# Optimization experiments

Hardware: AMD Instinct MI355X
Metric: run time of the kernel (lower is better)

Reference implementation:

```python
import jax, jax.numpy as jnp
import numpy as np

B, N, DIM = 8, 1024, 1024
HEADS, DIM_HEAD = 16, 64
INNER = HEADS * DIM_HEAD  # 1024


def setup_inputs() -> dict:
    key = jax.random.key(0)
    k1, k2, k3 = jax.random.split(key, 3)
    x = jax.random.normal(k1, (B, N, DIM), dtype=jnp.float32)
    # Dense kernels (Glorot-ish scale for numerical sanity)
    w_qkv = jax.random.normal(k2, (DIM, 3 * INNER), dtype=jnp.float32) * (DIM ** -0.5)
    w_out = jax.random.normal(k3, (INNER, DIM), dtype=jnp.float32) * (INNER ** -0.5)
    b_out = jnp.zeros((DIM,), dtype=jnp.float32)
    return {"x": x, "w_qkv": w_qkv, "w_out": w_out, "b_out": b_out}


def reference(x, w_qkv, w_out, b_out):
    scale = DIM_HEAD ** -0.5
    qkv = x @ w_qkv                                   # [B, N, 3*INNER]
    q, k, v = jnp.split(qkv, 3, axis=-1)              # each [B, N, INNER]

    def to_heads(t):
        # [B, N, H*Dh] -> [B, H, N, Dh]
        return t.reshape(B, N, HEADS, DIM_HEAD).transpose(0, 2, 1, 3)

    q, k, v = to_heads(q), to_heads(k), to_heads(v)
    dots = jnp.einsum("bhid,bhjd->bhij", q, k) * scale   # [B, H, N, N]
    attn = jax.nn.softmax(dots, axis=-1)
    out = jnp.einsum("bhij,bhjd->bhid", attn, v)          # [B, H, N, Dh]
    out = out.transpose(0, 2, 1, 3).reshape(B, N, INNER)  # merge heads
    return out @ w_out + b_out                            # project_out (dropout inactive at inference)
```

## Files before the change

### kernel.cpp

```cpp
#include <hip/hip_runtime.h>
#include <hip/hip_bf16.h>
#include <math.h>

typedef __bf16 bf16_t;
typedef __bf16 bf16x2 __attribute__((ext_vector_type(2)));
typedef __bf16 bf16x4 __attribute__((ext_vector_type(4)));
typedef __bf16 bf16x8 __attribute__((ext_vector_type(8)));
typedef float f32x4 __attribute__((ext_vector_type(4)));
typedef float f32x16 __attribute__((ext_vector_type(16)));

#define LOG2E 1.44269504088896340736f

#define GL2LDS(g, l)                                                     \
  __builtin_amdgcn_global_load_lds(                                      \
      (const __attribute__((address_space(1))) unsigned int*)(g),        \
      (__attribute__((address_space(3))) unsigned int*)(l), 16, 0, 0)

#define BAR() asm volatile("s_barrier" ::: "memory")
#define VMCNT(n) asm volatile("s_waitcnt vmcnt(" #n ")" ::: "memory")
#define LGKM0()                                         \
  do {                                                  \
    asm volatile("s_waitcnt lgkmcnt(0)" ::: "memory");  \
    __builtin_amdgcn_sched_barrier(0);                  \
  } while (0)

static __device__ __forceinline__ unsigned pk2(bf16_t a, bf16_t b) {
  bf16x2 t;
  t[0] = a;
  t[1] = b;
  return __builtin_bit_cast(unsigned, t);
}

__global__ __launch_bounds__(256) void convert_f32_bf16(const float* __restrict__ in,
                                                        bf16_t* __restrict__ out) {
  const size_t idx = (size_t)(blockIdx.x * 256 + threadIdx.x) * 8;
  f32x4 a = *(const f32x4*)&in[idx];
  f32x4 b = *(const f32x4*)&in[idx + 4];
  bf16x8 v;
#pragma unroll
  for (int i = 0; i < 4; i++) { v[i] = (bf16_t)a[i]; v[i + 4] = (bf16_t)b[i]; }
  *(bf16x8*)&out[idx] = v;
}

__global__ __launch_bounds__(256) void transpose_f32_bf16(const float* __restrict__ in,
                                                          bf16_t* __restrict__ out,
                                                          int R, int C) {
  __shared__ bf16_t t[64][65];
  const int c0 = blockIdx.x * 64, r0 = blockIdx.y * 64;
  const int tx = threadIdx.x, ty = threadIdx.y;
#pragma unroll
  for (int i = 0; i < 16; i++) {
    int r = ty + i * 4;
    t[r][tx] = (bf16_t)in[(size_t)(r0 + r) * C + c0 + tx];
  }
  __syncthreads();
#pragma unroll
  for (int i = 0; i < 16; i++) {
    int r = ty + i * 4;
    out[(size_t)(c0 + r) * R + r0 + tx] = t[tx][r];
  }
}

template <int MODE>
__global__ __launch_bounds__(256, 4) void gemmT(const bf16_t* __restrict__ A,
                                                const bf16_t* __restrict__ Bt,
                                                bf16_t* __restrict__ Qb,
                                                bf16_t* __restrict__ Kb,
                                                bf16_t* __restrict__ Vtb,
                                                const float* __restrict__ bias,
                                                float* __restrict__ Out) {
  constexpr int K = 1024;
  constexpr int NT = K / 32;
  __shared__ __align__(16) bf16_t As[3][128 * 32];
  __shared__ __align__(16) bf16_t Bs[3][128 * 32];
  const int gx = gridDim.x;
  const int lin = blockIdx.y * gx + blockIdx.x;
  const int per = (gx * gridDim.y) >> 3;
  const int swz = (lin & 7) * per + (lin >> 3);
  const int m0 = (swz / gx) * 128, n0 = (swz % gx) * 128;
  const int tid = threadIdx.x;
  const int w = tid >> 6, l = tid & 63;
  const int lr = l & 15, lq = l >> 4;
  const int wm = w >> 1, wn = w & 1;

  const int rs = tid >> 2, ps = tid & 3;
  const int cs = (ps ^ ((rs >> 1) & 3)) * 8;
  const size_t gA0 = (size_t)(m0 + rs) * K + cs;
  const size_t gA1 = (size_t)(m0 + 64 + rs) * K + cs;
  const size_t gB0 = (size_t)(n0 + rs) * K + cs;
  const size_t gB1 = (size_t)(n0 + 64 + rs) * K + cs;
  const int ldsu0 = (w * 64) * 8;
  const int ldsu1 = (256 + w * 64) * 8;

#define STG(bf_, kt_)                                   \
  do {                                                  \
    const size_t kk_ = (size_t)(kt_) * 32;              \
    GL2LDS(&A[gA0 + kk_], &As[bf_][ldsu0]);             \
    GL2LDS(&A[gA1 + kk_], &As[bf_][ldsu1]);             \
    GL2LDS(&Bt[gB0 + kk_], &Bs[bf_][ldsu0]);            \
    GL2LDS(&Bt[gB1 + kk_], &Bs[bf_][ldsu1]);            \
  } while (0)

  int aoff[4], boff[4];
#pragma unroll
  for (int mf = 0; mf < 4; mf++) {
    const int row = wm * 64 + mf * 16 + lr;
    aoff[mf] = row * 32 + ((lq ^ ((row >> 1) & 3)) << 3);
  }
#pragma unroll
  for (int nf = 0; nf < 4; nf++) {
    const int row = wn * 64 + nf * 16 + lr;
    boff[nf] = row * 32 + ((lq ^ ((row >> 1) & 3)) << 3);
  }

  f32x4 acc[4][4] = {};

  STG(0, 0);
  STG(1, 1);
  VMCNT(4);
  BAR();

  for (int t = 0; t < NT; ++t) {
    const int bufR = t % 3;
    if (t + 2 < NT) STG((t + 2) % 3, t + 2);
    bf16x8 af[4], bv[4];
#pragma unroll
    for (int mf = 0; mf < 4; mf++)
      af[mf] = *(const bf16x8*)&As[bufR][aoff[mf]];
#pragma unroll
    for (int nf = 0; nf < 4; nf++)
      bv[nf] = *(const bf16x8*)&Bs[bufR][boff[nf]];
    LGKM0();
    __builtin_amdgcn_s_setprio(1);
#pragma unroll
    for (int mf = 0; mf < 4; mf++)
#pragma unroll
      for (int nf = 0; nf < 4; nf++)
        acc[mf][nf] = __builtin_amdgcn_mfma_f32_16x16x32_bf16(af[mf], bv[nf],
                                                              acc[mf][nf], 0, 0, 0);
    __builtin_amdgcn_s_setprio(0);
    if (t == NT - 2) { VMCNT(0); } else if (t < NT - 2) { VMCNT(4); }
    BAR();
  }

#pragma unroll
  for (int mf = 0; mf < 4; mf++)
#pragma unroll
    for (int nf = 0; nf < 4; nf++)
#pragma unroll
      for (int i = 0; i < 4; i++) {
        const int m = m0 + wm * 64 + mf * 16 + lq * 4 + i;
        const int c = n0 + wn * 64 + nf * 16 + lr;
        const float v = acc[mf][nf][i];
        if (MODE == 1) {
          Out[(size_t)m * 1024 + c] = v + bias[c];
        } else {
          const int b = m >> 10, n = m & 1023;
          const int which = c >> 10, cc = c & 1023;
          const int hh = cc >> 6, d = cc & 63;
          const size_t qk = ((size_t)((b * 16 + hh) * 1024 + n)) * 64 + d;
          if (which == 0)
            Qb[qk] = (bf16_t)(v * (0.125f * LOG2E));
          else if (which == 1)
            Kb[qk] = (bf16_t)v;
          else
            Vtb[((size_t)((b * 16 + hh) * 64 + d)) * 1024 + n] = (bf16_t)v;
        }
      }
}

__global__ __launch_bounds__(256) void attn128(const bf16_t* __restrict__ Qb,
                                               const bf16_t* __restrict__ Kb,
                                               const bf16_t* __restrict__ Vtb,
                                               bf16_t* __restrict__ Ob) {
  __shared__ __align__(16) bf16_t Ks[2][64 * 64];
  __shared__ __align__(16) bf16_t Vs[2][64 * 64];
  const int bid = blockIdx.x;
  const int qt = bid >> 7, b = (bid >> 4) & 7, h = bid & 15;
  const bf16_t* Qh = Qb + (size_t)((b * 16 + h) * 1024) * 64;
  const bf16_t* Kh = Kb + (size_t)((b * 16 + h) * 1024) * 64;
  const bf16_t* Vh = Vtb + (size_t)((b * 16 + h) * 64) * 1024;
  const int tid = threadIdx.x, w = tid >> 6, l = tid & 63;
  const int lq31 = l & 31, hi = l >> 5;
  const int q0w = qt * 128 + w * 32;
  const int ksw = lq31 & 7;

  const int r0 = tid >> 3, p0 = tid & 7;
  const int ck = (p0 ^ (r0 & 7)) * 8;
  const int ldsS0 = (w * 64) * 8;
  const int ldsS1 = (256 + w * 64) * 8;

#define STGKV(bf_, j_)                                                  \
  do {                                                                  \
    const size_t jb = (size_t)(j_) * 64;                                \
    GL2LDS(&Kh[(jb + r0) * 64 + ck], &Ks[bf_][ldsS0]);                  \
    GL2LDS(&Kh[(jb + r0 + 32) * 64 + ck], &Ks[bf_][ldsS1]);             \
    GL2LDS(&Vh[(size_t)r0 * 1024 + jb + ck], &Vs[bf_][ldsS0]);          \
    GL2LDS(&Vh[(size_t)(r0 + 32) * 1024 + jb + ck], &Vs[bf_][ldsS1]);   \
  } while (0)

  bf16x8 qf[4];
#pragma unroll
  for (int c = 0; c < 4; c++)
    qf[c] = *(const bf16x8*)&Qh[(size_t)(q0w + lq31) * 64 + c * 16 + hi * 8];

  STGKV(0, 0);
  VMCNT(0);
  BAR();

  f32x16 o0 = {}, o1 = {};
  float denom = 0.0f;

  for (int it = 0; it < 16; ++it) {
    const int buf = it & 1;
    if (it < 15) STGKV(buf ^ 1, it + 1);
    f32x16 s0 = {}, s1 = {};
    __builtin_amdgcn_s_setprio(1);
#pragma unroll
    for (int c = 0; c < 4; c++) {
      const int col = ((c * 2 + hi) ^ ksw) << 3;
      bf16x8 kf0 = *(const bf16x8*)&Ks[buf][lq31 * 64 + col];
      bf16x8 kf1 = *(const bf16x8*)&Ks[buf][(32 + lq31) * 64 + col];
      s0 = __builtin_amdgcn_mfma_f32_32x32x16_bf16(kf0, qf[c], s0, 0, 0, 0);
      s1 = __builtin_amdgcn_mfma_f32_32x32x16_bf16(kf1, qf[c], s1, 0, 0, 0);
    }
    __builtin_amdgcn_s_setprio(0);
    unsigned wds[16];
    float dl = 0.0f;
#pragma unroll
    for (int j = 0; j < 8; j++) {
      bf16_t e0 = (bf16_t)exp2f(s0[2 * j]), e1 = (bf16_t)exp2f(s0[2 * j + 1]);
      dl += (float)e0 + (float)e1;
      wds[j] = pk2(e0, e1);
    }
#pragma unroll
    for (int j = 0; j < 8; j++) {
      bf16_t e0 = (bf16_t)exp2f(s1[2 * j]), e1 = (bf16_t)exp2f(s1[2 * j + 1]);
      dl += (float)e0 + (float)e1;
      wds[8 + j] = pk2(e0, e1);
    }
    denom += dl + __shfl_xor(dl, 32);
    bf16x8 pf[4];
#pragma unroll
    for (int q2 = 0; q2 < 4; q2++) {
      const int base = (q2 >> 1) * 8 + (q2 & 1) * 4;
      const unsigned a0 = wds[base], a1 = wds[base + 1];
      const unsigned a2 = wds[base + 2], a3 = wds[base + 3];
      const unsigned x0 = __shfl_xor(a0, 32), x1 = __shfl_xor(a1, 32);
      const unsigned x2 = __shfl_xor(a2, 32), x3 = __shfl_xor(a3, 32);
      union { unsigned u[4]; bf16x8 v; } u;
      u.u[0] = hi ? x2 : a0;
      u.u[1] = hi ? x3 : a1;
      u.u[2] = hi ? a2 : x0;
      u.u[3] = hi ? a3 : x1;
      pf[q2] = u.v;
    }
    __builtin_amdgcn_s_setprio(1);
#pragma unroll
    for (int c = 0; c < 4; c++) {
      const int col = ((c * 2 + hi) ^ ksw) << 3;
      bf16x8 vf0 = *(const bf16x8*)&Vs[buf][lq31 * 64 + col];
      bf16x8 vf1 = *(const bf16x8*)&Vs[buf][(32 + lq31) * 64 + col];
      o0 = __builtin_amdgcn_mfma_f32_32x32x16_bf16(vf0, pf[c], o0, 0, 0, 0);
      o1 = __builtin_amdgcn_mfma_f32_32x32x16_bf16(vf1, pf[c], o1, 0, 0, 0);
    }
    __builtin_amdgcn_s_setprio(0);
    VMCNT(0);
    BAR();
  }
  const float inv = 1.0f / denom;
  const int grow = b * 1024 + q0w + lq31;
#pragma unroll
  for (int db = 0; db < 2; db++)
#pragma unroll
    for (int rg = 0; rg < 4; rg++) {
      bf16x4 ov;
#pragma unroll
      for (int i = 0; i < 4; i++)
        ov[i] = (bf16_t)((db ? o1[rg * 4 + i] : o0[rg * 4 + i]) * inv);
      *(bf16x4*)&Ob[(size_t)grow * 1024 + h * 64 + db * 32 + rg * 8 + hi * 4] = ov;
    }
}

extern "C" void kernel_launch(void* const* d_in, const int* in_sizes, int n_in,
                              void* d_out, int out_size, void* d_ws, size_t ws_size,
                              hipStream_t stream) {
  const float* x     = (const float*)d_in[0];
  const float* w_qkv = (const float*)d_in[1];
  const float* w_out = (const float*)d_in[2];
  const float* b_out = (const float*)d_in[3];
  float* out = (float*)d_out;

  bf16_t* ws = (bf16_t*)d_ws;
  const size_t SZ = (size_t)8 * 1024 * 1024;
  bf16_t* Qb  = ws;
  bf16_t* Kb  = Qb + SZ;
  bf16_t* Vtb = Kb + SZ;
  bf16_t* Ob  = Vtb + SZ;
  bf16_t* Wqt = Ob + SZ;
  bf16_t* Wot = Wqt + (size_t)3072 * 1024;
  bf16_t* Xb  = Ob;

  hipLaunchKernelGGL(convert_f32_bf16, dim3(4096), dim3(256), 0, stream, x, Xb);
  hipLaunchKernelGGL(transpose_f32_bf16, dim3(48, 16), dim3(64, 4), 0, stream,
                     w_qkv, Wqt, 1024, 3072);
  hipLaunchKernelGGL(transpose_f32_bf16, dim3(16, 16), dim3(64, 4), 0, stream,
                     w_out, Wot, 1024, 1024);
  hipLaunchKernelGGL((gemmT<0>), dim3(24, 64), dim3(256), 0, stream,
                     Xb, Wqt, Qb, Kb, Vtb, (const float*)nullptr, (float*)nullptr);
  hipLaunchKernelGGL(attn128, dim3(1024), dim3(256), 0, stream, Qb, Kb, Vtb, Ob);
  hipLaunchKernelGGL((gemmT<1>), dim3(8, 64), dim3(256), 0, stream,
                     Ob, Wot, (bf16_t*)nullptr, (bf16_t*)nullptr, (bf16_t*)nullptr,
                     b_out, out);
}
```

Before: 285.9 us.

## Load GEMM A operand directly into registers and ring-buffer only B in LDS

The projection GEMM no longer stages the A tile through shared memory. Each wave loads its A fragments straight from global memory into double-buffered registers one k-step ahead. B stays on the async global-to-LDS path, now as a 4-deep ring, and the k-loop is unrolled by 4 so the buffer indices are compile-time constants. The aim is to cut LDS traffic and footprint, but A is now fetched twice, once by each wn wave, with less coalesced 16-byte row-strided accesses, and it relies on the compiler's vmcnt handling for the register loads.

Result: slower. 591.9 us (+107.1%).

```diff
diff --git a/kernel.cpp b/kernel.cpp
--- a/kernel.cpp
+++ b/kernel.cpp
@@ -71,8 +71,7 @@
                                                 float* __restrict__ Out) {
   constexpr int K = 1024;
   constexpr int NT = K / 32;
-  __shared__ __align__(16) bf16_t As[3][128 * 32];
-  __shared__ __align__(16) bf16_t Bs[3][128 * 32];
+  __shared__ __align__(16) bf16_t Bs[4][128 * 32];
   const int gx = gridDim.x;
   const int lin = blockIdx.y * gx + blockIdx.x;
   const int per = (gx * gridDim.y) >> 3;
@@ -85,28 +84,26 @@
 
   const int rs = tid >> 2, ps = tid & 3;
   const int cs = (ps ^ ((rs >> 1) & 3)) * 8;
-  const size_t gA0 = (size_t)(m0 + rs) * K + cs;
-  const size_t gA1 = (size_t)(m0 + 64 + rs) * K + cs;
   const size_t gB0 = (size_t)(n0 + rs) * K + cs;
   const size_t gB1 = (size_t)(n0 + 64 + rs) * K + cs;
   const int ldsu0 = (w * 64) * 8;
   const int ldsu1 = (256 + w * 64) * 8;
 
-#define STG(bf_, kt_)                                   \
+#define STGB(bf_, kt_)                                  \
   do {                                                  \
     const size_t kk_ = (size_t)(kt_) * 32;              \
-    GL2LDS(&A[gA0 + kk_], &As[bf_][ldsu0]);             \
-    GL2LDS(&A[gA1 + kk_], &As[bf_][ldsu1]);             \
     GL2LDS(&Bt[gB0 + kk_], &Bs[bf_][ldsu0]);            \
     GL2LDS(&Bt[gB1 + kk_], &Bs[bf_][ldsu1]);            \
   } while (0)
 
-  int aoff[4], boff[4];
-#pragma unroll
-  for (int mf = 0; mf < 4; mf++) {
-    const int row = wm * 64 + mf * 16 + lr;
-    aoff[mf] = row * 32 + ((lq ^ ((row >> 1) & 3)) << 3);
-  }
+  const bf16_t* Ab = &A[(size_t)(m0 + wm * 64 + lr) * K + lq * 8];
+#define LDA(dst_, kt_)                                            \
+  do {                                                            \
+    _Pragma("unroll") for (int mf_ = 0; mf_ < 4; mf_++)           \
+        (dst_)[mf_] = *(const bf16x8*)&Ab[(size_t)mf_ * 16 * K + (kt_) * 32]; \
+  } while (0)
+
+  int boff[4];
 #pragma unroll
   for (int nf = 0; nf < 4; nf++) {
     const int row = wn * 64 + nf * 16 + lr;
@@ -114,33 +111,36 @@
   }
 
   f32x4 acc[4][4] = {};
-
-  STG(0, 0);
-  STG(1, 1);
-  VMCNT(4);
+  bf16x8 afr[2][4];
+
+  STGB(0, 0);
+  LDA(afr[0], 0);
+  STGB(1, 1);
+  VMCNT(2);
   BAR();
 
-  for (int t = 0; t < NT; ++t) {
-    const int bufR = t % 3;
-    if (t + 2 < NT) STG((t + 2) % 3, t + 2);
-    bf16x8 af[4], bv[4];
-#pragma unroll
-    for (int mf = 0; mf < 4; mf++)
-      af[mf] = *(const bf16x8*)&As[bufR][aoff[mf]];
-#pragma unroll
-    for (int nf = 0; nf < 4; nf++)
-      bv[nf] = *(const bf16x8*)&Bs[bufR][boff[nf]];
-    LGKM0();
-    __builtin_amdgcn_s_setprio(1);
-#pragma unroll
-    for (int mf = 0; mf < 4; mf++)
+  for (int tb = 0; tb < NT; tb += 4) {
+#pragma unroll
+    for (int s = 0; s < 4; s++) {
+      const int t = tb + s;
+      if (t + 1 < NT) LDA(afr[(s + 1) & 1], t + 1);
+      if (t + 2 < NT) STGB((s + 2) & 3, t + 2);
+      bf16x8 bv[4];
 #pragma unroll
       for (int nf = 0; nf < 4; nf++)
-        acc[mf][nf] = __builtin_amdgcn_mfma_f32_16x16x32_bf16(af[mf], bv[nf],
-                                                              acc[mf][nf], 0, 0, 0);
-    __builtin_amdgcn_s_setprio(0);
-    if (t == NT - 2) { VMCNT(0); } else if (t < NT - 2) { VMCNT(4); }
-    BAR();
+        bv[nf] = *(const bf16x8*)&Bs[s][boff[nf]];
+      LGKM0();
+      __builtin_amdgcn_s_setprio(1);
+#pragma unroll
+      for (int mf = 0; mf < 4; mf++)
+#pragma unroll
+        for (int nf = 0; nf < 4; nf++)
+          acc[mf][nf] = __builtin_amdgcn_mfma_f32_16x16x32_bf16(
+              afr[s & 1][mf], bv[nf], acc[mf][nf], 0, 0, 0);
+      __builtin_amdgcn_s_setprio(0);
+      if (t < NT - 2) { VMCNT(2); } else if (t == NT - 2) { VMCNT(0); }
+      BAR();
+    }
   }
 
 #pragma unroll
```
